# Optimization experiments

Hardware: AMD Instinct MI355X
Metric: run time of the kernel (lower is better)

The kernel has to match this reference:

```python
import jax, jax.numpy as jnp
import numpy as np

B, HI, WI = 4, 24, 24
T = HI * WI
H, N = 12, 64
C = H * N
D_MIX, D_DECAY, D_AAA, D_KKK, D_GATE, D_MA, D_MK = 32, 64, 16, 16, 128, 16, 16


def q_shift(x, Hi, Wi):
    # 4-direction quarter-channel spatial shift (groups_q_shift, K=1, gamma=1/4)
    Bb, Nn, Cc = x.shape
    q = Cc // 4
    x4 = x.reshape(Bb, Hi, Wi, Cc)
    pad = lambda a, pw: jnp.pad(a, ((0, 0),) + pw + ((0, 0),))
    s1 = pad(x4[:, :, :-1, 0:q], ((0, 0), (1, 0)))        # shift right along W
    s2 = pad(x4[:, :, 1:, q:2 * q], ((0, 0), (0, 1)))     # shift left along W
    s3 = pad(x4[:, :-1, :, 2 * q:3 * q], ((1, 0), (0, 0)))  # shift down along H
    s4 = pad(x4[:, 1:, :, 3 * q:4 * q], ((0, 1), (0, 0)))   # shift up along H
    return jnp.concatenate([s1, s2, s3, s4], axis=-1).reshape(Bb, Nn, Cc)


def wkv7(r, w, k, v, a, b):
    # RWKV-7 delta-rule recurrence: S = S*diag(exp(w)) + S@(a b^T) + v k^T ; y = S r
    Bb, Tt, Cc = r.shape
    tohead = lambda t: t.reshape(Bb, Tt, H, N).transpose(1, 0, 2, 3)  # (T,B,H,N)
    rt, kt, vt, at, bt = map(tohead, (r, k, v, a, b))
    dt = jnp.exp(tohead(w))  # per-channel decay in (0, e^-0.5]

    def step(S, inp):
        r_, d_, k_, v_, a_, b_ = inp
        sa = jnp.einsum('bhij,bhj->bhi', S, a_)
        S = S * d_[:, :, None, :] + sa[..., None] * b_[:, :, None, :] + v_[..., None] * k_[:, :, None, :]
        return S, jnp.einsum('bhij,bhj->bhi', S, r_)

    S0 = jnp.zeros((Bb, H, N, N), r.dtype)
    _, ys = jax.lax.scan(step, S0, (rt, dt, kt, vt, at, bt))
    return ys.transpose(1, 0, 2, 3).reshape(Bb, Tt, Cc)


def group_norm(x, scale, bias, eps=64e-5):
    Bb, Tt, Cc = x.shape
    xg = x.reshape(Bb, Tt, H, N)
    mu = xg.mean(-1, keepdims=True)
    var = ((xg - mu) ** 2).mean(-1, keepdims=True)
    xn = ((xg - mu) * jax.lax.rsqrt(var + eps)).reshape(Bb, Tt, Cc)
    return xn * scale + bias


def fwd(x, maa_x, maa_rg, maa_wa, maa_k, maa_v, maa_w1, maa_w2,
        w0, wd1, wd2, a0, a1, a2, kk1, kk2, g1, g2,
        ma0, ma1, ma2, mk0, mk1, mk2, faaaa,
        Wr, Wk, Wv, Wo, ln_s, ln_b, h_img, w_img):
    Bb, Tt, Cc = x.shape
    xx = q_shift(x, h_img, w_img) - x
    xxx = x + xx * maa_x
    lora = jnp.tanh(xxx @ maa_w1).reshape(Bb, Tt, 4, D_MIX)
    m = jnp.einsum('btfd,fdc->fbtc', lora, maa_w2)  # (4,B,T,C)
    xrg = x + xx * (maa_rg + m[0])
    xwa = x + xx * (maa_wa + m[1])
    xk = x + xx * (maa_k + m[2])
    xv = x + xx * (maa_v + m[3])
    r = xrg @ Wr.T
    w = -jax.nn.softplus(-(w0 + jnp.tanh(xwa @ wd1) @ wd2)) - 0.5  # log-decay <= -0.5
    k = xk @ Wk.T
    v = xv @ Wv.T
    g = jax.nn.sigmoid(xrg @ g1) @ g2
    kk = k + jnp.tanh(xk @ kk1) @ kk2
    kkh = kk.reshape(Bb, Tt, H, N)
    kk = (kkh / jnp.maximum(jnp.linalg.norm(kkh, axis=-1, keepdims=True), 1e-12)).reshape(Bb, Tt, Cc)
    a = jax.nn.sigmoid(a0 + (xwa @ a1) @ a2)
    ma = jax.nn.sigmoid(ma0 + (xwa @ ma1) @ ma2)
    k = k * ma + k * a * (1.0 - ma)
    mk = jax.nn.sigmoid(mk0 + (xwa @ mk1) @ mk2)
    k = k * jnp.exp(jnp.minimum(w * mk, 0.0))
    y = wkv7(r, w, k, v, -kk, kk * a)
    y = group_norm(y, ln_s, ln_b)
    rh, kh, vh = (t.reshape(Bb, Tt, H, N) for t in (r, k, v))
    y = y + ((rh * kh * faaaa).sum(-1, keepdims=True) * vh).reshape(Bb, Tt, Cc)
    return (y * g) @ Wo.T


def setup_inputs() -> dict:
    key = jax.random.key(0)
    ks = iter(jax.random.split(key, 40))
    rn = lambda shape, s=0.02: jax.random.normal(next(ks), shape, jnp.float32) * s
    return {
        'x': rn((B, T, C), 1.0),
        'maa_x': rn((1, 1, C), 0.5), 'maa_rg': rn((1, 1, C), 0.5),
        'maa_wa': rn((1, 1, C), 0.5), 'maa_k': rn((1, 1, C), 0.5), 'maa_v': rn((1, 1, C), 0.5),
        'maa_w1': rn((C, 4 * D_MIX)), 'maa_w2': rn((4, D_MIX, C), 0.1),
        'w0': rn((1, 1, C), 0.5) - 4.0,
        'wd1': rn((C, D_DECAY)), 'wd2': rn((D_DECAY, C), 0.1),
        'a0': rn((1, 1, C), 0.1), 'a1': rn((C, D_AAA)), 'a2': rn((D_AAA, C), 0.1),
        'kk1': rn((C, D_KKK)), 'kk2': rn((D_KKK, C), 0.1),
        'g1': rn((C, D_GATE), 0.1), 'g2': rn((D_GATE, C), 0.1),
        'ma0': rn((1, 1, C), 0.1), 'ma1': rn((C, D_MA)), 'ma2': rn((D_MA, C), 0.1),
        'mk0': rn((1, 1, C), 0.1), 'mk1': rn((C, D_MK)), 'mk2': rn((D_MK, C), 0.1),
        'faaaa': rn((1, 1, H, N), 0.1),
        'Wr': rn((C, C)), 'Wk': rn((C, C)), 'Wv': rn((C, C)), 'Wo': rn((C, C)),
        'ln_s': jnp.ones((C,), jnp.float32), 'ln_b': jnp.zeros((C,), jnp.float32),
        'h_img': HI, 'w_img': WI,
    }


def reference(x, maa_x, maa_rg, maa_wa, maa_k, maa_v, maa_w1, maa_w2,
              w0, wd1, wd2, a0, a1, a2, kk1, kk2, g1, g2,
              ma0, ma1, ma2, mk0, mk1, mk2, faaaa,
              Wr, Wk, Wv, Wo, ln_s, ln_b, h_img, w_img):
    return fwd(x, maa_x, maa_rg, maa_wa, maa_k, maa_v, maa_w1, maa_w2,
               w0, wd1, wd2, a0, a1, a2, kk1, kk2, g1, g2,
               ma0, ma1, ma2, mk0, mk1, mk2, faaaa,
               Wr, Wk, Wv, Wo, ln_s, ln_b, h_img, w_img)
```

## Files before the change

### kernel.cpp

```cpp
#include <hip/hip_runtime.h>
#include <stdint.h>

#define Hh 12
#define Cc 768
#define Tt 576
#define BTC 1769472L
#define HI_ 24
#define WI_ 24
#define CH 16
#define NCH 36
#define RB 16

typedef unsigned int uint;
typedef unsigned short ushort;
typedef __attribute__((ext_vector_type(8))) short short8;
typedef __attribute__((ext_vector_type(4))) float f32x4;

__device__ __forceinline__ ushort f2b(float f) {
  uint u = __float_as_uint(f);
  u += 0x7FFFu + ((u >> 16) & 1u);
  return (ushort)(u >> 16);
}
__device__ __forceinline__ float b2f(ushort h) { return __uint_as_float(((uint)h) << 16); }
__device__ __forceinline__ float sigm(float x) { return 1.0f / (1.0f + __expf(-x)); }

__device__ __forceinline__ float dppx1(float x) {
  return __int_as_float(__builtin_amdgcn_mov_dpp(__float_as_int(x), 0xB1, 0xF, 0xF, true));
}
__device__ __forceinline__ float dppx2(float x) {
  return __int_as_float(__builtin_amdgcn_mov_dpp(__float_as_int(x), 0x4E, 0xF, 0xF, true));
}
__device__ __forceinline__ float mir8(float x) {
  return __int_as_float(__builtin_amdgcn_mov_dpp(__float_as_int(x), 0x141, 0xF, 0xF, true));
}

#define PUT2(buf, i, SZ, vexpr)                      \
  {                                                  \
    float _v = (vexpr);                              \
    ushort _h = f2b(_v);                             \
    (buf)[i] = _h;                                   \
    (buf)[(long)(SZ) + (i)] = f2b(_v - b2f(_h));     \
  }

struct Seg {
  const ushort* Ah; const ushort* Al; const ushort* Bh; const ushort* Bl;
  float* C; ushort* O; const float* maap;
  long osz;
  int K, lda, ldb, ldc, nby, epi;
};
struct SegPack {
  Seg s[6];
  int cum[6];
  const float* x; const float* xx;
};

__global__ __launch_bounds__(256) void gemm_multi(SegPack P) {
  __shared__ ushort sAh[128][40], sAl[128][40], sBh[64][40], sBl[64][40];
  const int bid = blockIdx.x;
  int si = 0;
#pragma unroll
  for (int i = 1; i < 6; i++) si = (bid >= P.cum[i]) ? i : si;
  const Seg sg = P.s[si];
  const int local = bid - P.cum[si];
  const int bx = local / sg.nby;
  const int by = local - bx * sg.nby;
  const int bm = bx * 128, bn = by * 64;
  const int tid = threadIdx.x;
  const int wave = tid >> 6, lane = tid & 63;
  const int wm = (wave >> 1) * 64, wn = (wave & 1) * 32;
  const int srow = tid >> 2, scol = (tid & 3) * 8;
  const int fr = lane & 15, kg = (lane >> 4) * 8;
  f32x4 acc[4][2] = {};
  const int lda = sg.lda, ldb = sg.ldb;
  const ushort* aph = sg.Ah + (long)(bm + srow) * lda + scol;
  const ushort* apl = sg.Al + (long)(bm + srow) * lda + scol;
  const ushort* bph = sg.Bh + (long)(bn + srow) * ldb + scol;
  const ushort* bpl = sg.Bl + (long)(bn + srow) * ldb + scol;
  const long a64 = 64L * lda;
  for (int k0 = 0; k0 < sg.K; k0 += 32) {
    short8 avh0 = *(const short8*)(aph + k0);
    short8 avh1 = *(const short8*)(aph + a64 + k0);
    short8 avl0 = *(const short8*)(apl + k0);
    short8 avl1 = *(const short8*)(apl + a64 + k0);
    short8 bvh0 = *(const short8*)(bph + k0);
    short8 bvl0 = *(const short8*)(bpl + k0);
    __syncthreads();
    *(short8*)&sAh[srow][scol] = avh0;
    *(short8*)&sAh[srow + 64][scol] = avh1;
    *(short8*)&sAl[srow][scol] = avl0;
    *(short8*)&sAl[srow + 64][scol] = avl1;
    *(short8*)&sBh[srow][scol] = bvh0;
    *(short8*)&sBl[srow][scol] = bvl0;
    __syncthreads();
    short8 bfh[2], bfl[2];
#pragma unroll
    for (int ni = 0; ni < 2; ni++) {
      bfh[ni] = *(const short8*)&sBh[wn + ni * 16 + fr][kg];
      bfl[ni] = *(const short8*)&sBl[wn + ni * 16 + fr][kg];
    }
#pragma unroll
    for (int mi = 0; mi < 4; mi++) {
      short8 afh = *(const short8*)&sAh[wm + mi * 16 + fr][kg];
      short8 afl = *(const short8*)&sAl[wm + mi * 16 + fr][kg];
#pragma unroll
      for (int ni = 0; ni < 2; ni++) {
        acc[mi][ni] = __builtin_amdgcn_mfma_f32_16x16x32_bf16(afh, bfh[ni], acc[mi][ni], 0, 0, 0);
        acc[mi][ni] = __builtin_amdgcn_mfma_f32_16x16x32_bf16(afh, bfl[ni], acc[mi][ni], 0, 0, 0);
        acc[mi][ni] = __builtin_amdgcn_mfma_f32_16x16x32_bf16(afl, bfh[ni], acc[mi][ni], 0, 0, 0);
      }
    }
  }
  const int row4 = (lane >> 4) * 4;
  const int ldc = sg.ldc;
  if (sg.epi == 0) {
#pragma unroll
    for (int mi = 0; mi < 4; mi++)
#pragma unroll
      for (int ni = 0; ni < 2; ni++) {
        int gc = bn + wn + ni * 16 + fr;
        long base = (long)(bm + wm + mi * 16 + row4) * ldc + gc;
#pragma unroll
        for (int rr = 0; rr < 4; rr++) sg.C[base + (long)rr * ldc] = acc[mi][ni][rr];
      }
  } else if (sg.epi == 3) {
#pragma unroll
    for (int mi = 0; mi < 4; mi++)
#pragma unroll
      for (int ni = 0; ni < 2; ni++) {
        int gc = bn + wn + ni * 16 + fr;
        long base = (long)(bm + wm + mi * 16 + row4) * 768 + gc;
        float mc = sg.maap[gc];
#pragma unroll
        for (int rr = 0; rr < 4; rr++) {
          long ix = base + (long)rr * 768;
          float xv = P.x[ix], d = P.xx[ix];
          PUT2(sg.O, ix, sg.osz, xv + d * (mc + acc[mi][ni][rr]));
        }
      }
  } else {
    const bool istanh = (sg.epi == 1);
#pragma unroll
    for (int mi = 0; mi < 4; mi++)
#pragma unroll
      for (int ni = 0; ni < 2; ni++) {
        int gc = bn + wn + ni * 16 + fr;
        long base = (long)(bm + wm + mi * 16 + row4) * ldc + gc;
#pragma unroll
        for (int rr = 0; rr < 4; rr++) {
          float v = acc[mi][ni][rr];
          v = istanh ? tanhf(v) : sigm(v);
          PUT2(sg.O, base + (long)rr * ldc, sg.osz, v);
        }
      }
  }
}

__global__ __launch_bounds__(256) void conv_bigw(const float* __restrict__ Wr,
                                                 const float* __restrict__ Wk,
                                                 const float* __restrict__ Wv,
                                                 const float* __restrict__ Wo,
                                                 ushort* __restrict__ Wb) {
  long idx = (long)blockIdx.x * 256 + threadIdx.x;
  const long WSZ = 589824;
  int seg = (int)(idx / WSZ);
  long off = idx % WSZ;
  const float* s = (seg == 0) ? Wr : (seg == 1) ? Wk : (seg == 2) ? Wv : Wo;
  PUT2(Wb, idx, 2359296L, s[off]);
}

__global__ __launch_bounds__(256) void prep_smallw(
    const float* maa_w1, const float* maa_w2, const float* wd1, const float* wd2,
    const float* a1, const float* a2, const float* kk1, const float* kk2,
    const float* g1, const float* g2, const float* ma1, const float* ma2,
    const float* mk1, const float* mk2, ushort* w1T, ushort* w2T, ushort* wcat1,
    ushort* kk1T, ushort* g1T, ushort* wd2T, ushort* armk2T, ushort* g2T) {
  int idx = blockIdx.x * 256 + threadIdx.x;
  if (idx < 98304) { int n = idx / 768, c = idx % 768; PUT2(w1T, idx, 98304, maa_w1[c * 128 + n]); return; }
  idx -= 98304;
  if (idx < 98304) {
    int f = idx / 24576, r = idx % 24576; int n = r / 32, d = r % 32;
    PUT2(w2T, idx, 98304, maa_w2[(f * 32 + d) * 768 + n]); return;
  }
  idx -= 98304;
  if (idx < 49152) { int n = idx / 768, c = idx % 768; PUT2(wcat1, idx, 98304, wd1[c * 64 + n]); return; }
  idx -= 49152;
  if (idx < 12288) { int n = idx / 768, c = idx % 768; PUT2(wcat1, 49152 + idx, 98304, a1[c * 16 + n]); return; }
  idx -= 12288;
  if (idx < 12288) { int n = idx / 768, c = idx % 768; PUT2(wcat1, 61440 + idx, 98304, ma1[c * 16 + n]); return; }
  idx -= 12288;
  if (idx < 12288) { int n = idx / 768, c = idx % 768; PUT2(wcat1, 73728 + idx, 98304, mk1[c * 16 + n]); return; }
  idx -= 12288;
  if (idx < 12288) { wcat1[86016 + idx] = 0; wcat1[98304 + 86016 + idx] = 0; return; }
  idx -= 12288;
  if (idx < 12288) { int n = idx / 768, c = idx % 768; PUT2(kk1T, idx, 49152, kk1[c * 16 + n]); return; }
  idx -= 12288;
  if (idx < 36864) { kk1T[12288 + idx] = 0; kk1T[49152 + 12288 + idx] = 0; return; }
  idx -= 36864;
  if (idx < 98304) { int n = idx / 768, c = idx % 768; PUT2(g1T, idx, 98304, g1[c * 128 + n]); return; }
  idx -= 98304;
  if (idx < 49152) { int n = idx / 64, d = idx % 64; PUT2(wd2T, idx, 49152, wd2[d * 768 + n]); return; }
  idx -= 49152;
  if (idx < 98304) {
    int f = idx / 24576, r = idx % 24576; int n = r / 32, d = r % 32;
    const float* s = (f == 0) ? a2 : (f == 1) ? ma2 : (f == 2) ? mk2 : kk2;
    float v = (d < 16) ? s[d * 768 + n] : 0.0f;
    PUT2(armk2T, idx, 98304, v); return;
  }
  idx -= 98304;
  if (idx < 98304) { int n = idx / 128, d = idx % 128; PUT2(g2T, idx, 98304, g2[d * 768 + n]); }
}

__global__ __launch_bounds__(256) void qshift_mix(const float* __restrict__ x,
                                                  const float* __restrict__ maa_x,
                                                  float* __restrict__ xx,
                                                  ushort* __restrict__ xxxs) {
  long idx = (long)blockIdx.x * 256 + threadIdx.x;
  int c = (int)(idx % Cc);
  int bt = (int)(idx / Cc);
  int t = bt % Tt;
  int hh = t / WI_, ww = t % WI_;
  int q = c / 192;
  float s = 0.f;
  if (q == 0) { if (ww > 0) s = x[idx - Cc]; }
  else if (q == 1) { if (ww < WI_ - 1) s = x[idx + Cc]; }
  else if (q == 2) { if (hh > 0) s = x[idx - (long)WI_ * Cc]; }
  else { if (hh < HI_ - 1) s = x[idx + (long)WI_ * Cc]; }
  float xv = x[idx];
  float d = s - xv;
  xx[idx] = d;
  PUT2(xxxs, idx, BTC, xv + d * maa_x[c]);
}

__global__ __launch_bounds__(256) void build_a2(const float* __restrict__ wlora,
                                                const float* __restrict__ kklora,
                                                ushort* __restrict__ A2s) {
  int idx = blockIdx.x * 256 + threadIdx.x;
  int bt = idx / 160, col = idx % 160;
  float v;
  if (col < 64) v = tanhf(wlora[bt * 128 + col]);
  else if (col < 112) v = wlora[bt * 128 + col];
  else if (col < 128) v = tanhf(kklora[bt * 64 + (col - 112)]);
  else v = 0.0f;
  PUT2(A2s, idx, 368640, v);
}

__global__ __launch_bounds__(256) void post_rwkv(
    const float* __restrict__ k, const float* __restrict__ wraw, const float* __restrict__ w0,
    const float* __restrict__ a0, const float* __restrict__ ma0, const float* __restrict__ mk0,
    float* araw, float* maraw, float* mkraw, float* kkraw) {
  int gw = blockIdx.x * 4 + (threadIdx.x >> 6);
  int j = threadIdx.x & 63;
  int bt = gw / Hh, h = gw % Hh;
  int c = h * 64 + j;
  long idx = (long)bt * Cc + c;
  float kv = k[idx];
  float kkv = kv + kkraw[idx];
  float ss = kkv * kkv;
  for (int mm = 1; mm < 64; mm <<= 1) ss += __shfl_xor(ss, mm, 64);
  float rn = 1.0f / fmaxf(sqrtf(ss), 1e-12f);
  float kkn = kkv * rn;
  float z = w0[c] + wraw[idx];
  float w = fminf(z, 0.f) - log1pf(__expf(-fabsf(z))) - 0.5f;
  float a = sigm(a0[c] + araw[idx]);
  float ma = sigm(ma0[c] + maraw[idx]);
  float mk = sigm(mk0[c] + mkraw[idx]);
  float k2 = kv * ma + kv * a * (1.f - ma);
  float k3 = k2 * __expf(fminf(w * mk, 0.f));
  araw[idx] = -kkn;
  maraw[idx] = kkn * a;
  mkraw[idx] = __expf(w);
  kkraw[idx] = k3;
}

__global__ __launch_bounds__(128, 1) void wkv7(const float* __restrict__ r,
                                               const float* __restrict__ dd,
                                               const float* __restrict__ kk,
                                               const float* __restrict__ vv,
                                               const float* __restrict__ aa,
                                               const float* __restrict__ bb,
                                               float* __restrict__ y) {
  __shared__ float sc[2][5][CH][64];
  __shared__ float sv[2][CH][RB];
  const int blk = blockIdx.x;
  const int bh = blk >> 2;
  const int rb = blk & 3;
  const int b = bh / Hh, h = bh % Hh;
  const int tid = threadIdx.x;
  const int wave = tid >> 6, lane = tid & 63;
  const int rl = lane >> 3, cg = lane & 7;
  const int row = rb * RB + wave * 8 + rl;
  const int cb = cg * 8;
  const int vri = wave * 8 + rl;
  const long vecbase = ((long)b * Tt) * Cc + h * 64;
  float* py = y + vecbase + row;
  const float* gp[5] = {r, dd, kk, aa, bb};
  float S[8];
#pragma unroll
  for (int u = 0; u < 8; u++) S[u] = 0.f;
  f32x4 gq[10];
  float gv[2];
  f32x4 Xq[10], Yq[10];
  float Xv, Yv;

#define SLOAD(t0)                                                              \
  {                                                                            \
    _Pragma("unroll") for (int q = 0; q < 10; q++) {                           \
      const int arr = q >> 1;                                                  \
      const int i2 = ((q & 1) << 7) + tid;                                     \
      gq[q] = *(const f32x4*)(gp[arr] + vecbase + (long)((t0) + (i2 >> 4)) * Cc \
                              + ((i2 & 15) << 2));                             \
    }                                                                          \
    _Pragma("unroll") for (int j = 0; j < 2; j++) {                            \
      const int i2 = (j << 7) + tid;                                           \
      gv[j] = vv[vecbase + (long)((t0) + (i2 >> 4)) * Cc + rb * RB + (i2 & 15)]; \
    }                                                                          \
  }
#define SWRITE(bi)                                                             \
  {                                                                            \
    _Pragma("unroll") for (int q = 0; q < 10; q++) {                           \
      const int i2 = ((q & 1) << 7) + tid;                                     \
      *(f32x4*)&sc[bi][q >> 1][i2 >> 4][(i2 & 15) << 2] = gq[q];               \
    }                                                                          \
    _Pragma("unroll") for (int j = 0; j < 2; j++) {                            \
      const int i2 = (j << 7) + tid;                                           \
      sv[bi][i2 >> 4][i2 & 15] = gv[j];                                        \
    }                                                                          \
  }
#define LREAD(Q, Vv_, pb, t)                                                   \
  {                                                                            \
    Q[0] = *(const f32x4*)&sc[pb][3][t][cb];                                   \
    Q[1] = *(const f32x4*)&sc[pb][3][t][cb + 4];                               \
    Q[2] = *(const f32x4*)&sc[pb][1][t][cb];                                   \
    Q[3] = *(const f32x4*)&sc[pb][1][t][cb + 4];                               \
    Q[4] = *(const f32x4*)&sc[pb][2][t][cb];                                   \
    Q[5] = *(const f32x4*)&sc[pb][2][t][cb + 4];                               \
    Q[6] = *(const f32x4*)&sc[pb][4][t][cb];                                   \
    Q[7] = *(const f32x4*)&sc[pb][4][t][cb + 4];                               \
    Q[8] = *(const f32x4*)&sc[pb][0][t][cb];                                   \
    Q[9] = *(const f32x4*)&sc[pb][0][t][cb + 4];                               \
    Vv_ = sv[pb][t][vri];                                                      \
  }
#define WCOMP(Q, Vv_, yoff)                                                    \
  {                                                                            \
    float p0 = S[0] * Q[0][0] + S[4] * Q[1][0];                                \
    float p1 = S[1] * Q[0][1] + S[5] * Q[1][1];                                \
    float p2 = S[2] * Q[0][2] + S[6] * Q[1][2];                                \
    float p3 = S[3] * Q[0][3] + S[7] * Q[1][3];                                \
    float sa = (p0 + p1) + (p2 + p3);                                          \
    sa += dppx1(sa); sa += dppx2(sa); sa += mir8(sa);                          \
    float q0, q1, q2, q3;                                                      \
    S[0] = fmaf(S[0], Q[2][0], fmaf(sa, Q[6][0], Vv_ * Q[4][0])); q0 = S[0] * Q[8][0]; \
    S[1] = fmaf(S[1], Q[2][1], fmaf(sa, Q[6][1], Vv_ * Q[4][1])); q1 = S[1] * Q[8][1]; \
    S[2] = fmaf(S[2], Q[2][2], fmaf(sa, Q[6][2], Vv_ * Q[4][2])); q2 = S[2] * Q[8][2]; \
    S[3] = fmaf(S[3], Q[2][3], fmaf(sa, Q[6][3], Vv_ * Q[4][3])); q3 = S[3] * Q[8][3]; \
    S[4] = fmaf(S[4], Q[3][0], fmaf(sa, Q[7][0], Vv_ * Q[5][0])); q0 += S[4] * Q[9][0]; \
    S[5] = fmaf(S[5], Q[3][1], fmaf(sa, Q[7][1], Vv_ * Q[5][1])); q1 += S[5] * Q[9][1]; \
    S[6] = fmaf(S[6], Q[3][2], fmaf(sa, Q[7][2], Vv_ * Q[5][2])); q2 += S[6] * Q[9][2]; \
    S[7] = fmaf(S[7], Q[3][3], fmaf(sa, Q[7][3], Vv_ * Q[5][3])); q3 += S[7] * Q[9][3]; \
    float yp = (q0 + q1) + (q2 + q3);                                          \
    yp += dppx1(yp); yp += dppx2(yp); yp += mir8(yp);                          \
    if (cg == 0) py[yoff] = yp;                                                \
  }

  SLOAD(0);
  SWRITE(0);
  __syncthreads();
  SLOAD(CH);
  for (int ch = 0; ch < NCH; ch++) {
    const int pb = ch & 1;
    const long ybase = (long)ch * CH * Cc;
    LREAD(Xq, Xv, pb, 0);
#pragma unroll
    for (int t = 0; t < CH; t += 2) {
      LREAD(Yq, Yv, pb, t + 1);
      WCOMP(Xq, Xv, ybase + (long)t * Cc);
      if (t + 2 < CH) LREAD(Xq, Xv, pb, t + 2);
      WCOMP(Yq, Yv, ybase + (long)(t + 1) * Cc);
    }
    __syncthreads();
    if (ch + 1 < NCH) {
      SWRITE(pb ^ 1);
      if (ch + 2 < NCH) SLOAD((ch + 2) * CH);
    }
    __syncthreads();
  }
#undef SLOAD
#undef SWRITE
#undef LREAD
#undef WCOMP
}

__global__ __launch_bounds__(256) void gn_bonus_gate(
    const float* __restrict__ y, const float* __restrict__ r, const float* __restrict__ k3,
    const float* __restrict__ v, const float* __restrict__ g, const float* __restrict__ faaaa,
    const float* __restrict__ lns, const float* __restrict__ lnb, ushort* __restrict__ ygs) {
  int gw = blockIdx.x * 4 + (threadIdx.x >> 6);
  int j = threadIdx.x & 63;
  int bt = gw / Hh, h = gw % Hh;
  int c = h * 64 + j;
  long idx = (long)bt * Cc + c;
  float yv = y[idx];
  float s1 = yv, s2 = yv * yv;
  float s3 = r[idx] * k3[idx] * faaaa[c];
  for (int mm = 1; mm < 64; mm <<= 1) {
    s1 += __shfl_xor(s1, mm, 64);
    s2 += __shfl_xor(s2, mm, 64);
    s3 += __shfl_xor(s3, mm, 64);
  }
  float mu = s1 * (1.f / 64.f);
  float var = s2 * (1.f / 64.f) - mu * mu;
  float xn = (yv - mu) * rsqrtf(var + 64e-5f);
  float y2 = xn * lns[c] + lnb[c] + s3 * v[idx];
  PUT2(ygs, idx, BTC, y2 * g[idx]);
}

extern "C" void kernel_launch(void* const* d_in, const int* in_sizes, int n_in,
                              void* d_out, int out_size, void* d_ws, size_t ws_size,
                              hipStream_t stream) {
  const float* x = (const float*)d_in[0];
  const float* maa_x = (const float*)d_in[1];
  const float* maa_rg = (const float*)d_in[2];
  const float* maa_wa = (const float*)d_in[3];
  const float* maa_k = (const float*)d_in[4];
  const float* maa_v = (const float*)d_in[5];
  const float* maa_w1 = (const float*)d_in[6];
  const float* maa_w2 = (const float*)d_in[7];
  const float* w0 = (const float*)d_in[8];
  const float* wd1 = (const float*)d_in[9];
  const float* wd2 = (const float*)d_in[10];
  const float* a0 = (const float*)d_in[11];
  const float* a1 = (const float*)d_in[12];
  const float* a2 = (const float*)d_in[13];
  const float* kk1 = (const float*)d_in[14];
  const float* kk2 = (const float*)d_in[15];
  const float* g1 = (const float*)d_in[16];
  const float* g2 = (const float*)d_in[17];
  const float* ma0 = (const float*)d_in[18];
  const float* ma1 = (const float*)d_in[19];
  const float* ma2 = (const float*)d_in[20];
  const float* mk0 = (const float*)d_in[21];
  const float* mk1 = (const float*)d_in[22];
  const float* mk2 = (const float*)d_in[23];
  const float* faaaa = (const float*)d_in[24];
  const float* Wr = (const float*)d_in[25];
  const float* Wk = (const float*)d_in[26];
  const float* Wv = (const float*)d_in[27];
  const float* Wo = (const float*)d_in[28];
  const float* lns = (const float*)d_in[29];
  const float* lnb = (const float*)d_in[30];

  float* fw = (float*)d_ws;
  float* xx = fw;
  float* m = fw + BTC;
  float* rbuf = fw + 5 * BTC;
  float* kbuf = fw + 6 * BTC;
  float* vbuf = fw + 7 * BTC;
  float* wrawb = fw + 8 * BTC;
  float* gbuf = fw + 9 * BTC;
  float* ybuf = fw + 10 * BTC;
  float* wlora = fw + 11 * BTC;
  float* kklora = wlora + 294912;
  ushort* ub = (ushort*)(kklora + 147456);
  ushort* xxxs = ub;   ub += 2 * BTC;
  ushort* x4s = ub;    ub += 8 * BTC;
  ushort* lts = ub;    ub += 2 * 294912;
  ushort* A2s = ub;    ub += 2 * 368640;
  ushort* glss = ub;   ub += 2 * 294912;
  ushort* ygs = ub;    ub += 2 * BTC;
  ushort* Wb = ub;     ub += 2 * 2359296L;
  ushort* w1T = ub;    ub += 2 * 98304;
  ushort* w2T = ub;    ub += 2 * 98304;
  ushort* wcat1 = ub;  ub += 2 * 98304;
  ushort* kk1T = ub;   ub += 2 * 49152;
  ushort* g1T = ub;    ub += 2 * 98304;
  ushort* wd2T = ub;   ub += 2 * 49152;
  ushort* armk2T = ub; ub += 2 * 98304;
  ushort* g2T = ub;    ub += 2 * 98304;

  const int IMAX = 0x7fffffff;
  dim3 blk(256);
  conv_bigw<<<9216, blk, 0, stream>>>(Wr, Wk, Wv, Wo, Wb);
  prep_smallw<<<2688, blk, 0, stream>>>(maa_w1, maa_w2, wd1, wd2, a1, a2, kk1, kk2, g1, g2,
                                        ma1, ma2, mk1, mk2, w1T, w2T, wcat1, kk1T, g1T, wd2T,
                                        armk2T, g2T);
  qshift_mix<<<6912, blk, 0, stream>>>(x, maa_x, xx, xxxs);

  {
    SegPack P = {};
    P.s[0] = {xxxs, xxxs + BTC, w1T, w1T + 98304, nullptr, lts, nullptr,
              294912, 768, 768, 768, 128, 2, 1};
    P.cum[0] = 0;
    for (int i = 1; i < 6; i++) P.cum[i] = IMAX;
    P.x = x; P.xx = xx;
    gemm_multi<<<36, blk, 0, stream>>>(P);
  }
  {
    SegPack P = {};
    const float* maaps[4] = {maa_rg, maa_wa, maa_k, maa_v};
    const int planes[4] = {0, 3, 1, 2};
    for (int f = 0; f < 4; f++) {
      P.s[f] = {lts + f * 32, lts + 294912 + f * 32, w2T + f * 24576,
                w2T + 98304 + f * 24576, nullptr, x4s + (long)planes[f] * BTC, maaps[f],
                4 * BTC, 32, 128, 32, 768, 12, 3};
      P.cum[f] = f * 216;
    }
    for (int i = 4; i < 6; i++) P.cum[i] = IMAX;
    P.x = x; P.xx = xx;
    gemm_multi<<<864, blk, 0, stream>>>(P);
  }
  {
    SegPack P = {};
    for (int f = 0; f < 3; f++) {
      float* cout = (f == 0) ? rbuf : (f == 1) ? kbuf : vbuf;
      P.s[f] = {x4s + (long)f * BTC, x4s + (long)(4 + f) * BTC, Wb + (long)f * 589824,
                Wb + 2359296L + (long)f * 589824, cout, nullptr, nullptr,
                0, 768, 768, 768, 768, 12, 0};
      P.cum[f] = f * 216;
    }
    P.s[3] = {x4s + 3 * BTC, x4s + 7 * BTC, wcat1, wcat1 + 98304, wlora, nullptr, nullptr,
              0, 768, 768, 768, 128, 2, 0};
    P.cum[3] = 648;
    P.s[4] = {x4s, x4s + 4 * BTC, g1T, g1T + 98304, nullptr, glss, nullptr,
              294912, 768, 768, 768, 128, 2, 2};
    P.cum[4] = 684;
    P.s[5] = {x4s + BTC, x4s + 5 * BTC, kk1T, kk1T + 49152, kklora, nullptr, nullptr,
              0, 768, 768, 768, 64, 1, 0};
    P.cum[5] = 720;
    P.x = x; P.xx = xx;
    gemm_multi<<<738, blk, 0, stream>>>(P);
  }
  build_a2<<<1440, blk, 0, stream>>>(wlora, kklora, A2s);
  {
    SegPack P = {};
    P.s[0] = {A2s, A2s + 368640, wd2T, wd2T + 49152, wrawb, nullptr, nullptr,
              0, 64, 160, 64, 768, 12, 0};
    P.cum[0] = 0;
    for (int f = 0; f < 4; f++) {
      P.s[1 + f] = {A2s + 64 + 16 * f, A2s + 368640 + 64 + 16 * f, armk2T + f * 24576,
                    armk2T + 98304 + f * 24576, m + (long)f * BTC, nullptr, nullptr,
                    0, 32, 160, 32, 768, 12, 0};
      P.cum[1 + f] = 216 + f * 216;
    }
    P.s[5] = {glss, glss + 294912, g2T, g2T + 98304, gbuf, nullptr, nullptr,
              0, 128, 128, 128, 768, 12, 0};
    P.cum[5] = 1080;
    P.x = x; P.xx = xx;
    gemm_multi<<<1296, blk, 0, stream>>>(P);
  }
  post_rwkv<<<6912, blk, 0, stream>>>(kbuf, wrawb, w0, a0, ma0, mk0,
                                      m, m + BTC, m + 2 * BTC, m + 3 * BTC);
  wkv7<<<192, dim3(128), 0, stream>>>(rbuf, m + 2 * BTC, m + 3 * BTC, vbuf, m, m + BTC, ybuf);
  gn_bonus_gate<<<6912, blk, 0, stream>>>(ybuf, rbuf, m + 3 * BTC, vbuf, gbuf, faaaa,
                                          lns, lnb, ygs);
  {
    SegPack P = {};
    P.s[0] = {ygs, ygs + BTC, Wb + 3L * 589824, Wb + 2359296L + 3L * 589824,
              (float*)d_out, nullptr, nullptr, 0, 768, 768, 768, 768, 12, 0};
    P.cum[0] = 0;
    for (int i = 1; i < 6; i++) P.cum[i] = IMAX;
    P.x = x; P.xx = xx;
    gemm_multi<<<216, blk, 0, stream>>>(P);
  }
}
```

Before: 395.0 us.

## Run wkv7 with one wave per block, two state rows per lane

The WKV7 recurrence kernel now uses a single 64-lane wave per block instead of two waves, and each lane keeps two state rows (S0, S1) rather than one. The shared-memory chunk of r/w/k/a/b is read once and reused for both rows, and the two reduction chains are interleaved to expose instruction-level parallelism. The global-to-shared staging loads are reorganised for 64 threads, with v fetched as one vector per lane. The aim is fewer LDS reads per unit of state work and cheaper block barriers, at the cost of more registers per lane and half as many waves in flight on the 192 blocks.

After: 438.9 us. 1.11x slower.

```diff
diff --git a/kernel.cpp b/kernel.cpp
--- a/kernel.cpp
+++ b/kernel.cpp
@@ -272,61 +272,54 @@
   kkraw[idx] = k3;
 }
 
-__global__ __launch_bounds__(128, 1) void wkv7(const float* __restrict__ r,
-                                               const float* __restrict__ dd,
-                                               const float* __restrict__ kk,
-                                               const float* __restrict__ vv,
-                                               const float* __restrict__ aa,
-                                               const float* __restrict__ bb,
-                                               float* __restrict__ y) {
+__global__ __launch_bounds__(64, 1) void wkv7(const float* __restrict__ r,
+                                              const float* __restrict__ dd,
+                                              const float* __restrict__ kk,
+                                              const float* __restrict__ vv,
+                                              const float* __restrict__ aa,
+                                              const float* __restrict__ bb,
+                                              float* __restrict__ y) {
   __shared__ float sc[2][5][CH][64];
-  __shared__ float sv[2][CH][RB];
+  __shared__ float sv[2][CH][16];
   const int blk = blockIdx.x;
   const int bh = blk >> 2;
   const int rb = blk & 3;
   const int b = bh / Hh, h = bh % Hh;
-  const int tid = threadIdx.x;
-  const int wave = tid >> 6, lane = tid & 63;
+  const int lane = threadIdx.x;
   const int rl = lane >> 3, cg = lane & 7;
-  const int row = rb * RB + wave * 8 + rl;
   const int cb = cg * 8;
-  const int vri = wave * 8 + rl;
   const long vecbase = ((long)b * Tt) * Cc + h * 64;
-  float* py = y + vecbase + row;
+  float* py0 = y + vecbase + rb * 16 + rl;
+  float* py1 = py0 + 8;
   const float* gp[5] = {r, dd, kk, aa, bb};
-  float S[8];
-#pragma unroll
-  for (int u = 0; u < 8; u++) S[u] = 0.f;
-  f32x4 gq[10];
-  float gv[2];
+  float S0[8], S1[8];
+#pragma unroll
+  for (int u = 0; u < 8; u++) { S0[u] = 0.f; S1[u] = 0.f; }
+  f32x4 gq[20];
+  f32x4 gv;
   f32x4 Xq[10], Yq[10];
-  float Xv, Yv;
+  float Xv0, Xv1, Yv0, Yv1;
 
 #define SLOAD(t0)                                                              \
   {                                                                            \
-    _Pragma("unroll") for (int q = 0; q < 10; q++) {                           \
-      const int arr = q >> 1;                                                  \
-      const int i2 = ((q & 1) << 7) + tid;                                     \
+    _Pragma("unroll") for (int q = 0; q < 20; q++) {                           \
+      const int arr = q >> 2;                                                  \
+      const int i2 = ((q & 3) << 6) + lane;                                    \
       gq[q] = *(const f32x4*)(gp[arr] + vecbase + (long)((t0) + (i2 >> 4)) * Cc \
                               + ((i2 & 15) << 2));                             \
     }                                                                          \
-    _Pragma("unroll") for (int j = 0; j < 2; j++) {                            \
-      const int i2 = (j << 7) + tid;                                           \
-      gv[j] = vv[vecbase + (long)((t0) + (i2 >> 4)) * Cc + rb * RB + (i2 & 15)]; \
-    }                                                                          \
+    gv = *(const f32x4*)(vv + vecbase + (long)((t0) + (lane >> 2)) * Cc        \
+                         + rb * 16 + ((lane & 3) << 2));                       \
   }
 #define SWRITE(bi)                                                             \
   {                                                                            \
-    _Pragma("unroll") for (int q = 0; q < 10; q++) {                           \
-      const int i2 = ((q & 1) << 7) + tid;                                     \
-      *(f32x4*)&sc[bi][q >> 1][i2 >> 4][(i2 & 15) << 2] = gq[q];               \
+    _Pragma("unroll") for (int q = 0; q < 20; q++) {                           \
+      const int i2 = ((q & 3) << 6) + lane;                                    \
+      *(f32x4*)&sc[bi][q >> 2][i2 >> 4][(i2 & 15) << 2] = gq[q];               \
     }                                                                          \
-    _Pragma("unroll") for (int j = 0; j < 2; j++) {                            \
-      const int i2 = (j << 7) + tid;                                           \
-      sv[bi][i2 >> 4][i2 & 15] = gv[j];                                        \
-    }                                                                          \
-  }
-#define LREAD(Q, Vv_, pb, t)                                                   \
+    *(f32x4*)&sv[bi][lane >> 2][(lane & 3) << 2] = gv;                         \
+  }
+#define LREAD(Q, V0_, V1_, pb, t)                                              \
   {                                                                            \
     Q[0] = *(const f32x4*)&sc[pb][3][t][cb];                                   \
     Q[1] = *(const f32x4*)&sc[pb][3][t][cb + 4];                               \
@@ -338,28 +331,47 @@
     Q[7] = *(const f32x4*)&sc[pb][4][t][cb + 4];                               \
     Q[8] = *(const f32x4*)&sc[pb][0][t][cb];                                   \
     Q[9] = *(const f32x4*)&sc[pb][0][t][cb + 4];                               \
-    Vv_ = sv[pb][t][vri];                                                      \
-  }
-#define WCOMP(Q, Vv_, yoff)                                                    \
+    V0_ = sv[pb][t][rl];                                                       \
+    V1_ = sv[pb][t][rl + 8];                                                   \
+  }
+#define WCOMP(Q, V0_, V1_, yoff)                                               \
   {                                                                            \
-    float p0 = S[0] * Q[0][0] + S[4] * Q[1][0];                                \
-    float p1 = S[1] * Q[0][1] + S[5] * Q[1][1];                                \
-    float p2 = S[2] * Q[0][2] + S[6] * Q[1][2];                                \
-    float p3 = S[3] * Q[0][3] + S[7] * Q[1][3];                                \
-    float sa = (p0 + p1) + (p2 + p3);                                          \
-    sa += dppx1(sa); sa += dppx2(sa); sa += mir8(sa);                          \
-    float q0, q1, q2, q3;                                                      \
-    S[0] = fmaf(S[0], Q[2][0], fmaf(sa, Q[6][0], Vv_ * Q[4][0])); q0 = S[0] * Q[8][0]; \
-    S[1] = fmaf(S[1], Q[2][1], fmaf(sa, Q[6][1], Vv_ * Q[4][1])); q1 = S[1] * Q[8][1]; \
-    S[2] = fmaf(S[2], Q[2][2], fmaf(sa, Q[6][2], Vv_ * Q[4][2])); q2 = S[2] * Q[8][2]; \
-    S[3] = fmaf(S[3], Q[2][3], fmaf(sa, Q[6][3], Vv_ * Q[4][3])); q3 = S[3] * Q[8][3]; \
-    S[4] = fmaf(S[4], Q[3][0], fmaf(sa, Q[7][0], Vv_ * Q[5][0])); q0 += S[4] * Q[9][0]; \
-    S[5] = fmaf(S[5], Q[3][1], fmaf(sa, Q[7][1], Vv_ * Q[5][1])); q1 += S[5] * Q[9][1]; \
-    S[6] = fmaf(S[6], Q[3][2], fmaf(sa, Q[7][2], Vv_ * Q[5][2])); q2 += S[6] * Q[9][2]; \
-    S[7] = fmaf(S[7], Q[3][3], fmaf(sa, Q[7][3], Vv_ * Q[5][3])); q3 += S[7] * Q[9][3]; \
-    float yp = (q0 + q1) + (q2 + q3);                                          \
-    yp += dppx1(yp); yp += dppx2(yp); yp += mir8(yp);                          \
-    if (cg == 0) py[yoff] = yp;                                                \
+    float p00 = S0[0] * Q[0][0] + S0[4] * Q[1][0];                             \
+    float p01 = S0[1] * Q[0][1] + S0[5] * Q[1][1];                             \
+    float p02 = S0[2] * Q[0][2] + S0[6] * Q[1][2];                             \
+    float p03 = S0[3] * Q[0][3] + S0[7] * Q[1][3];                             \
+    float p10 = S1[0] * Q[0][0] + S1[4] * Q[1][0];                             \
+    float p11 = S1[1] * Q[0][1] + S1[5] * Q[1][1];                             \
+    float p12 = S1[2] * Q[0][2] + S1[6] * Q[1][2];                             \
+    float p13 = S1[3] * Q[0][3] + S1[7] * Q[1][3];                             \
+    float sa0 = (p00 + p01) + (p02 + p03);                                     \
+    float sa1 = (p10 + p11) + (p12 + p13);                                     \
+    sa0 += dppx1(sa0); sa1 += dppx1(sa1);                                      \
+    sa0 += dppx2(sa0); sa1 += dppx2(sa1);                                      \
+    sa0 += mir8(sa0);  sa1 += mir8(sa1);                                       \
+    float q00, q01, q02, q03, q10, q11, q12, q13;                              \
+    S0[0] = fmaf(S0[0], Q[2][0], fmaf(sa0, Q[6][0], V0_ * Q[4][0])); q00 = S0[0] * Q[8][0]; \
+    S0[1] = fmaf(S0[1], Q[2][1], fmaf(sa0, Q[6][1], V0_ * Q[4][1])); q01 = S0[1] * Q[8][1]; \
+    S0[2] = fmaf(S0[2], Q[2][2], fmaf(sa0, Q[6][2], V0_ * Q[4][2])); q02 = S0[2] * Q[8][2]; \
+    S0[3] = fmaf(S0[3], Q[2][3], fmaf(sa0, Q[6][3], V0_ * Q[4][3])); q03 = S0[3] * Q[8][3]; \
+    S0[4] = fmaf(S0[4], Q[3][0], fmaf(sa0, Q[7][0], V0_ * Q[5][0])); q00 += S0[4] * Q[9][0]; \
+    S0[5] = fmaf(S0[5], Q[3][1], fmaf(sa0, Q[7][1], V0_ * Q[5][1])); q01 += S0[5] * Q[9][1]; \
+    S0[6] = fmaf(S0[6], Q[3][2], fmaf(sa0, Q[7][2], V0_ * Q[5][2])); q02 += S0[6] * Q[9][2]; \
+    S0[7] = fmaf(S0[7], Q[3][3], fmaf(sa0, Q[7][3], V0_ * Q[5][3])); q03 += S0[7] * Q[9][3]; \
+    S1[0] = fmaf(S1[0], Q[2][0], fmaf(sa1, Q[6][0], V1_ * Q[4][0])); q10 = S1[0] * Q[8][0]; \
+    S1[1] = fmaf(S1[1], Q[2][1], fmaf(sa1, Q[6][1], V1_ * Q[4][1])); q11 = S1[1] * Q[8][1]; \
+    S1[2] = fmaf(S1[2], Q[2][2], fmaf(sa1, Q[6][2], V1_ * Q[4][2])); q12 = S1[2] * Q[8][2]; \
+    S1[3] = fmaf(S1[3], Q[2][3], fmaf(sa1, Q[6][3], V1_ * Q[4][3])); q13 = S1[3] * Q[8][3]; \
+    S1[4] = fmaf(S1[4], Q[3][0], fmaf(sa1, Q[7][0], V1_ * Q[5][0])); q10 += S1[4] * Q[9][0]; \
+    S1[5] = fmaf(S1[5], Q[3][1], fmaf(sa1, Q[7][1], V1_ * Q[5][1])); q11 += S1[5] * Q[9][1]; \
+    S1[6] = fmaf(S1[6], Q[3][2], fmaf(sa1, Q[7][2], V1_ * Q[5][2])); q12 += S1[6] * Q[9][2]; \
+    S1[7] = fmaf(S1[7], Q[3][3], fmaf(sa1, Q[7][3], V1_ * Q[5][3])); q13 += S1[7] * Q[9][3]; \
+    float yp0 = (q00 + q01) + (q02 + q03);                                     \
+    float yp1 = (q10 + q11) + (q12 + q13);                                     \
+    yp0 += dppx1(yp0); yp1 += dppx1(yp1);                                      \
+    yp0 += dppx2(yp0); yp1 += dppx2(yp1);                                      \
+    yp0 += mir8(yp0);  yp1 += mir8(yp1);                                       \
+    if (cg == 0) { py0[yoff] = yp0; py1[yoff] = yp1; }                         \
   }
 
   SLOAD(0);
@@ -369,13 +381,13 @@
   for (int ch = 0; ch < NCH; ch++) {
     const int pb = ch & 1;
     const long ybase = (long)ch * CH * Cc;
-    LREAD(Xq, Xv, pb, 0);
+    LREAD(Xq, Xv0, Xv1, pb, 0);
 #pragma unroll
     for (int t = 0; t < CH; t += 2) {
-      LREAD(Yq, Yv, pb, t + 1);
-      WCOMP(Xq, Xv, ybase + (long)t * Cc);
-      if (t + 2 < CH) LREAD(Xq, Xv, pb, t + 2);
-      WCOMP(Yq, Yv, ybase + (long)(t + 1) * Cc);
+      LREAD(Yq, Yv0, Yv1, pb, t + 1);
+      WCOMP(Xq, Xv0, Xv1, ybase + (long)t * Cc);
+      if (t + 2 < CH) LREAD(Xq, Xv0, Xv1, pb, t + 2);
+      WCOMP(Yq, Yv0, Yv1, ybase + (long)(t + 1) * Cc);
     }
     __syncthreads();
     if (ch + 1 < NCH) {
@@ -549,7 +561,7 @@
   }
   post_rwkv<<<6912, blk, 0, stream>>>(kbuf, wrawb, w0, a0, ma0, mk0,
                                       m, m + BTC, m + 2 * BTC, m + 3 * BTC);
-  wkv7<<<192, dim3(128), 0, stream>>>(rbuf, m + 2 * BTC, m + 3 * BTC, vbuf, m, m + BTC, ybuf);
+  wkv7<<<192, dim3(64), 0, stream>>>(rbuf, m + 2 * BTC, m + 3 * BTC, vbuf, m, m + BTC, ybuf);
   gn_bonus_gate<<<6912, blk, 0, stream>>>(ybuf, rbuf, m + 3 * BTC, vbuf, gbuf, faaaa,
                                           lns, lnb, ygs);
   {
```
